# Performance work log

Measured on AMD Instinct MI355X. Metric: run time of the kernel, lower is better.

Reference implementation:

```python
import jax, jax.numpy as jnp
import numpy as np
from jax import lax

B, H, OUT, STEPS = 256, 512, 9, 325  # 1 initial step + 325 unrolled steps = 326 outputs


def setup_inputs() -> dict:
    key = jax.random.key(0)
    ks = jax.random.split(key, 12)
    s = 0.05
    return {
        "x": jax.random.normal(ks[0], (B, H), jnp.float32),
        "hx0": jax.random.normal(ks[1], (B, H), jnp.float32),
        "cx0": jax.random.normal(ks[2], (B, H), jnp.float32),
        "W_ih": jax.random.normal(ks[3], (4 * H, H), jnp.float32) * s,
        "W_hh": jax.random.normal(ks[4], (4 * H, H), jnp.float32) * s,
        "b_ih": jax.random.normal(ks[5], (4 * H,), jnp.float32) * s,
        "b_hh": jax.random.normal(ks[6], (4 * H,), jnp.float32) * s,
        "W1": jax.random.normal(ks[7], (H, H), jnp.float32) * s,
        "b1": jax.random.normal(ks[8], (H,), jnp.float32) * s,
        "W2": jax.random.normal(ks[9], (OUT, H), jnp.float32) * s,
        "b2": jax.random.normal(ks[10], (OUT,), jnp.float32) * s,
    }


def reference(x, hx0, cx0, W_ih, W_hh, b_ih, b_hh, W1, b1, W2, b2):
    def lstm_cell(inp, h, c):
        # PyTorch LSTMCell gate order: i, f, g, o
        gates = inp @ W_ih.T + b_ih + h @ W_hh.T + b_hh  # [B, 4H]
        i, f, g, o = jnp.split(gates, 4, axis=-1)
        i = jax.nn.sigmoid(i)
        f = jax.nn.sigmoid(f)
        g = jnp.tanh(g)
        o = jax.nn.sigmoid(o)
        c_new = f * c + i * g
        h_new = o * jnp.tanh(c_new)
        return h_new, c_new

    def mlp(h):
        return jax.nn.relu(h @ W1.T + b1) @ W2.T + b2  # [B, 9]

    h, c = lstm_cell(x, hx0, cx0)
    y0 = mlp(h)

    def step(carry, _):
        h, c = carry
        # original: self.cell(hx, (hx, cx)) -- input IS the current hidden state
        h, c = lstm_cell(h, h, c)
        return (h, c), mlp(h)

    _, ys = lax.scan(step, (h, c), None, length=STEPS)  # ys: [325, B, 9]
    out = jnp.concatenate([y0[None], ys], axis=0)  # [326, B, 9]
    return jnp.transpose(out, (1, 0, 2))  # [B, 326, 9]
```

## Files before the change

kernel.cpp:

```cpp
#include <hip/hip_runtime.h>
#include <cstdio>

#define B_   256
#define H_   512
#define G4_  2048
#define T_   326
#define OUT_ 9

typedef __attribute__((ext_vector_type(8))) short s16x8;
typedef __attribute__((ext_vector_type(4))) float f32x4;

__device__ inline unsigned short to_bf16(float f) {
    unsigned int u = __builtin_bit_cast(unsigned int, f);
    unsigned int r = (u + 0x7fffu + ((u >> 16) & 1u)) >> 16;
    return (unsigned short)r;
}

__device__ inline float sigmoidf_(float x) { return 1.0f / (1.0f + __expf(-x)); }

__device__ inline float fast_tanh(float x) {
    x = fminf(fmaxf(x, -15.f), 15.f);
    float e = __expf(2.f * x);
    return (e - 1.f) / (e + 1.f);
}


__global__ void prep_weights(const float* __restrict__ Wih, const float* __restrict__ Whh,
                             const float* __restrict__ bih, const float* __restrict__ bhh,
                             unsigned short* __restrict__ Wc, unsigned short* __restrict__ Wcat,
                             float* __restrict__ bc) {
    int idx = blockIdx.x * 256 + threadIdx.x;
    int n = idx >> 9, k = idx & 511;
    float wi = Wih[idx], wh = Whh[idx];
    Wc[idx] = to_bf16(wi + wh);
    Wcat[(n << 10) + k]       = to_bf16(wi);
    Wcat[(n << 10) + 512 + k] = to_bf16(wh);
    if (k == 0) bc[n] = bih[n] + bhh[n];
}

__global__ void prep_w1(const float* __restrict__ W1, unsigned short* __restrict__ W1b) {
    int idx = blockIdx.x * 256 + threadIdx.x;
    W1b[idx] = to_bf16(W1[idx]);
}

__global__ void prep_w2(const float* __restrict__ W2, unsigned short* __restrict__ W2b) {
    int idx = blockIdx.x * 256 + threadIdx.x;
    int o = idx >> 9, k = idx & 511;
    W2b[idx] = (o < OUT_) ? to_bf16(W2[o * H_ + k]) : (unsigned short)0;
}

__global__ void prep_x(const float* __restrict__ x, const float* __restrict__ hx0,
                       unsigned short* __restrict__ xcat) {
    int idx = blockIdx.x * 256 + threadIdx.x;
    int b = idx >> 9, k = idx & 511;
    xcat[(b << 10) + k]       = to_bf16(x[idx]);
    xcat[(b << 10) + 512 + k] = to_bf16(hx0[idx]);
}

template <int KLEN>
__global__ __launch_bounds__(256) void lstm_step(
    const unsigned short* __restrict__ A,
    const unsigned short* __restrict__ W,
    const float* __restrict__ bc,
    const float* __restrict__ c_in,
    float* __restrict__ c_out,
    unsigned short* __restrict__ h_out) {
    const int lane = threadIdx.x & 63;
    const int wave = threadIdx.x >> 6;
    const int mn = lane & 15, q = lane >> 4;
    const int rt = blockIdx.x & 15;
    const int hb = (blockIdx.x >> 4) * 64 + wave * 16;

    const unsigned short* ap  = A + (size_t)(rt * 16 + mn) * KLEN + q * 8;
    const unsigned short* wp0 = W + (size_t)(0 * H_ + hb + mn) * KLEN + q * 8;
    const unsigned short* wp1 = W + (size_t)(1 * H_ + hb + mn) * KLEN + q * 8;
    const unsigned short* wp2 = W + (size_t)(2 * H_ + hb + mn) * KLEN + q * 8;
    const unsigned short* wp3 = W + (size_t)(3 * H_ + hb + mn) * KLEN + q * 8;

    f32x4 acc0 = {0.f,0.f,0.f,0.f}, acc1 = {0.f,0.f,0.f,0.f};
    f32x4 acc2 = {0.f,0.f,0.f,0.f}, acc3 = {0.f,0.f,0.f,0.f};
#pragma unroll 4
    for (int k0 = 0; k0 < KLEN; k0 += 32) {
        s16x8 a  = *reinterpret_cast<const s16x8*>(ap + k0);
        s16x8 w0 = *reinterpret_cast<const s16x8*>(wp0 + k0);
        s16x8 w1 = *reinterpret_cast<const s16x8*>(wp1 + k0);
        s16x8 w2 = *reinterpret_cast<const s16x8*>(wp2 + k0);
        s16x8 w3 = *reinterpret_cast<const s16x8*>(wp3 + k0);
        acc0 = __builtin_amdgcn_mfma_f32_16x16x32_bf16(a, w0, acc0, 0, 0, 0);
        acc1 = __builtin_amdgcn_mfma_f32_16x16x32_bf16(a, w1, acc1, 0, 0, 0);
        acc2 = __builtin_amdgcn_mfma_f32_16x16x32_bf16(a, w2, acc2, 0, 0, 0);
        acc3 = __builtin_amdgcn_mfma_f32_16x16x32_bf16(a, w3, acc3, 0, 0, 0);
    }

    const int j = hb + mn;
    const float bi = bc[j], bfv = bc[H_ + j], bg = bc[2 * H_ + j], bo = bc[3 * H_ + j];
#pragma unroll
    for (int r = 0; r < 4; ++r) {
        const int row = rt * 16 + q * 4 + r;
        const float iv = sigmoidf_(acc0[r] + bi);
        const float fv = sigmoidf_(acc1[r] + bfv);
        const float gv = fast_tanh(acc2[r] + bg);
        const float ov = sigmoidf_(acc3[r] + bo);
        const float co = c_in[row * H_ + j];
        const float cn = fv * co + iv * gv;
        c_out[row * H_ + j] = cn;
        h_out[row * H_ + j] = to_bf16(ov * fast_tanh(cn));
    }
}

__global__ __launch_bounds__(256) void lstm_persist(
    const unsigned short* __restrict__ Wc,
    const float* __restrict__ bc,
    const float* __restrict__ c0,
    unsigned short* __restrict__ h_hist,
    unsigned int* __restrict__ ctr) {
    __shared__ unsigned short A_lds[16 * 512];
    __shared__ float gate_lds[4 * 16 * 33];
    const int tid = threadIdx.x;
    const int lane = tid & 63, wave = tid >> 6;
    const int mn = lane & 15, q = lane >> 4;
    const int g  = blockIdx.x & 15;
    const int jb = (blockIdx.x >> 4) * 32;
    unsigned int* ctr_g = ctr + g * 32;

    s16x8 breg[2][16];
#pragma unroll
    for (int n = 0; n < 2; ++n) {
        const unsigned short* wp = Wc + (size_t)(wave * H_ + jb + n * 16 + mn) * H_ + q * 8;
#pragma unroll
        for (int kk = 0; kk < 16; ++kk)
            breg[n][kk] = *reinterpret_cast<const s16x8*>(wp + kk * 32);
    }
    const float bcv0 = bc[wave * H_ + jb + mn];
    const float bcv1 = bc[wave * H_ + jb + 16 + mn];

    const int crow = tid >> 4, cc0 = (tid & 15) * 2;
    float c_x = c0[(size_t)(g * 16 + crow) * H_ + jb + cc0];
    float c_y = c0[(size_t)(g * 16 + crow) * H_ + jb + cc0 + 1];

    int a_st[8];
#pragma unroll
    for (int p = 0; p < 8; ++p) {
        const int qi = p * 256 + tid;
        const int row = qi >> 7;
        const int bcol = (qi & 127) * 8;
        a_st[p] = row * 512 + (((bcol) ^ ((row & 7) << 4)) >> 1);
    }
    int a_rd[16];
#pragma unroll
    for (int kk = 0; kk < 16; ++kk) {
        const int bcol = kk * 64 + q * 16;
        a_rd[kk] = mn * 512 + ((bcol ^ ((mn & 7) << 4)) >> 1);
    }

    for (int t = 1; t < T_; ++t) {
        const unsigned long long* hsrc64 = reinterpret_cast<const unsigned long long*>(
            h_hist + (size_t)(t - 1) * (B_ * H_) + (size_t)g * 16 * H_);
        unsigned long long vv[8];
#pragma unroll
        for (int p = 0; p < 8; ++p)
            vv[p] = __hip_atomic_load(hsrc64 + p * 256 + tid, __ATOMIC_RELAXED,
                                      __HIP_MEMORY_SCOPE_AGENT);
#pragma unroll
        for (int p = 0; p < 8; ++p)
            *reinterpret_cast<unsigned long long*>(&A_lds[a_st[p]]) = vv[p];
        __syncthreads();

        f32x4 acc0 = {0.f,0.f,0.f,0.f}, acc1 = {0.f,0.f,0.f,0.f};
#pragma unroll
        for (int kk = 0; kk < 16; ++kk) {
            s16x8 a = *reinterpret_cast<const s16x8*>(&A_lds[a_rd[kk]]);
            acc0 = __builtin_amdgcn_mfma_f32_16x16x32_bf16(a, breg[0][kk], acc0, 0, 0, 0);
            acc1 = __builtin_amdgcn_mfma_f32_16x16x32_bf16(a, breg[1][kk], acc1, 0, 0, 0);
        }

#pragma unroll
        for (int r = 0; r < 4; ++r) {
            float v0 = acc0[r] + bcv0, v1 = acc1[r] + bcv1;
            if (wave == 2) { v0 = fast_tanh(v0); v1 = fast_tanh(v1); }
            else           { v0 = sigmoidf_(v0); v1 = sigmoidf_(v1); }
            gate_lds[(wave * 16 + (q * 4 + r)) * 33 + mn]      = v0;
            gate_lds[(wave * 16 + (q * 4 + r)) * 33 + 16 + mn] = v1;
        }
        __syncthreads();

        {
            float iv0 = gate_lds[(0 * 16 + crow) * 33 + cc0], iv1 = gate_lds[(0 * 16 + crow) * 33 + cc0 + 1];
            float fv0 = gate_lds[(1 * 16 + crow) * 33 + cc0], fv1 = gate_lds[(1 * 16 + crow) * 33 + cc0 + 1];
            float gv0 = gate_lds[(2 * 16 + crow) * 33 + cc0], gv1 = gate_lds[(2 * 16 + crow) * 33 + cc0 + 1];
            float ov0 = gate_lds[(3 * 16 + crow) * 33 + cc0], ov1 = gate_lds[(3 * 16 + crow) * 33 + cc0 + 1];
            c_x = fv0 * c_x + iv0 * gv0;
            c_y = fv1 * c_y + iv1 * gv1;
            unsigned int h0 = to_bf16(ov0 * fast_tanh(c_x));
            unsigned int h1 = to_bf16(ov1 * fast_tanh(c_y));
            unsigned int packed = h0 | (h1 << 16);
            unsigned int* hdst = reinterpret_cast<unsigned int*>(
                h_hist + (size_t)t * (B_ * H_) + (size_t)(g * 16 + crow) * H_ + jb + cc0);
            __hip_atomic_store(hdst, packed, __ATOMIC_RELAXED, __HIP_MEMORY_SCOPE_AGENT);
        }

        if (t < T_ - 1) {
            __syncthreads();
            asm volatile("" ::: "memory");
            if (tid == 0) {
                __hip_atomic_fetch_add(ctr_g, 1u, __ATOMIC_RELAXED, __HIP_MEMORY_SCOPE_AGENT);
                const unsigned int target = 16u * (unsigned int)t;
                while (__hip_atomic_load(ctr_g, __ATOMIC_RELAXED, __HIP_MEMORY_SCOPE_AGENT) < target) {
                }
            }
            asm volatile("" ::: "memory");
            __syncthreads();
        }
    }
}

__global__ __launch_bounds__(256) void mlp_kernel(
    const unsigned short* __restrict__ h_hist,
    const unsigned short* __restrict__ W1b,
    const float* __restrict__ b1,
    const unsigned short* __restrict__ W2b,
    const float* __restrict__ b2,
    float* __restrict__ out) {
    constexpr int ZS = 520;
    __shared__ unsigned short z_lds[32 * ZS];

    const int lane = threadIdx.x & 63;
    const int wave = threadIdx.x >> 6;
    const int mn = lane & 15, q = lane >> 4;
    const int t = blockIdx.x >> 2, mt = blockIdx.x & 3;

    const unsigned short* Abase = h_hist + ((size_t)t * B_ + mt * 64) * H_;
    const int nb = wave * 128;

    f32x4 zero4 = {0.f,0.f,0.f,0.f};
    f32x4 acc[4][8];
#pragma unroll
    for (int m4 = 0; m4 < 4; ++m4)
#pragma unroll
        for (int nt = 0; nt < 8; ++nt) acc[m4][nt] = zero4;

    for (int k0 = 0; k0 < 512; k0 += 32) {
        s16x8 a[4];
#pragma unroll
        for (int m4 = 0; m4 < 4; ++m4)
            a[m4] = *reinterpret_cast<const s16x8*>(Abase + (size_t)(m4 * 16 + mn) * H_ + k0 + q * 8);
#pragma unroll
        for (int nt = 0; nt < 8; ++nt) {
            s16x8 b = *reinterpret_cast<const s16x8*>(W1b + (size_t)(nb + nt * 16 + mn) * H_ + k0 + q * 8);
#pragma unroll
            for (int m4 = 0; m4 < 4; ++m4)
                acc[m4][nt] = __builtin_amdgcn_mfma_f32_16x16x32_bf16(a[m4], b, acc[m4][nt], 0, 0, 0);
        }
    }

    float b1v[8];
#pragma unroll
    for (int nt = 0; nt < 8; ++nt) b1v[nt] = b1[nb + nt * 16 + mn];

    for (int pass = 0; pass < 2; ++pass) {
        __syncthreads();
#pragma unroll
        for (int m4i = 0; m4i < 2; ++m4i) {
            const int m4 = 2 * pass + m4i;
            const int rl = m4i * 16 + q * 4;
#pragma unroll
            for (int nt = 0; nt < 8; ++nt) {
                const int col = nb + nt * 16 + mn;
#pragma unroll
                for (int r = 0; r < 4; ++r) {
                    float v = acc[m4][nt][r] + b1v[nt];
                    v = v > 0.f ? v : 0.f;
                    z_lds[(rl + r) * ZS + col] = to_bf16(v);
                }
            }
        }
        __syncthreads();
        if (wave < 2) {
            f32x4 yacc = {0.f,0.f,0.f,0.f};
#pragma unroll 4
            for (int k0 = 0; k0 < 512; k0 += 32) {
                s16x8 az = *reinterpret_cast<const s16x8*>(&z_lds[(wave * 16 + mn) * ZS + k0 + q * 8]);
                s16x8 bw = *reinterpret_cast<const s16x8*>(W2b + (size_t)mn * H_ + k0 + q * 8);
                yacc = __builtin_amdgcn_mfma_f32_16x16x32_bf16(az, bw, yacc, 0, 0, 0);
            }
            if (mn < OUT_) {
                const float bias = b2[mn];
#pragma unroll
                for (int r = 0; r < 4; ++r) {
                    const int row_local = pass * 32 + wave * 16 + q * 4 + r;
                    const int b = mt * 64 + row_local;
                    out[(size_t)b * (T_ * OUT_) + t * OUT_ + mn] = yacc[r] + bias;
                }
            }
        }
    }
}

extern "C" void kernel_launch(void* const* d_in, const int* in_sizes, int n_in,
                              void* d_out, int out_size, void* d_ws, size_t ws_size,
                              hipStream_t stream) {
    (void)in_sizes; (void)n_in; (void)out_size;
    const float* x   = (const float*)d_in[0];
    const float* hx0 = (const float*)d_in[1];
    const float* cx0 = (const float*)d_in[2];
    const float* Wih = (const float*)d_in[3];
    const float* Whh = (const float*)d_in[4];
    const float* bih = (const float*)d_in[5];
    const float* bhh = (const float*)d_in[6];
    const float* W1  = (const float*)d_in[7];
    const float* b1  = (const float*)d_in[8];
    const float* W2  = (const float*)d_in[9];
    const float* b2  = (const float*)d_in[10];
    float* out = (float*)d_out;

    char* p = (char*)d_ws;
    size_t off = 0;
    auto alloc = [&](size_t bytes) {
        void* r = p + off;
        off = (off + bytes + 255) & ~(size_t)255;
        return r;
    };
    unsigned short* Wc     = (unsigned short*)alloc((size_t)G4_ * H_ * 2);
    unsigned short* Wcat   = (unsigned short*)alloc((size_t)G4_ * 1024 * 2);
    unsigned short* W1b    = (unsigned short*)alloc((size_t)H_ * H_ * 2);
    unsigned short* W2b    = (unsigned short*)alloc((size_t)16 * H_ * 2);
    float*          bc     = (float*)alloc((size_t)G4_ * 4);
    unsigned short* xcat   = (unsigned short*)alloc((size_t)B_ * 1024 * 2);
    float*          cbuf   = (float*)alloc((size_t)B_ * H_ * 4);
    unsigned int*   ctr    = (unsigned int*)alloc(4096);
    unsigned short* h_hist = (unsigned short*)alloc((size_t)T_ * B_ * H_ * 2);
    if (off > ws_size) {
        fprintf(stderr, "kernel_launch: ws too small: need %zu have %zu\n", off, ws_size);
        return;
    }

    prep_weights<<<G4_ * H_ / 256, 256, 0, stream>>>(Wih, Whh, bih, bhh, Wc, Wcat, bc);
    prep_w1<<<H_ * H_ / 256, 256, 0, stream>>>(W1, W1b);
    prep_w2<<<16 * H_ / 256, 256, 0, stream>>>(W2, W2b);
    prep_x<<<B_ * H_ / 256, 256, 0, stream>>>(x, hx0, xcat);

    lstm_step<1024><<<128, 256, 0, stream>>>(xcat, Wcat, bc, cx0, cbuf, h_hist);

    hipMemsetAsync(ctr, 0, 4096, stream);
    {
        const unsigned short* Wc_l = Wc;
        const float* bc_l = bc;
        const float* c0_l = cbuf;
        unsigned short* hh_l = h_hist;
        unsigned int* ctr_l = ctr;
        void* args[5] = {(void*)&Wc_l, (void*)&bc_l, (void*)&c0_l, (void*)&hh_l, (void*)&ctr_l};
        hipLaunchCooperativeKernel((const void*)lstm_persist, dim3(256), dim3(256), args, 0, stream);
    }

    mlp_kernel<<<T_ * 4, 256, 0, stream>>>(h_hist, W1b, b1, W2b, b2, out);
}
```

Before: 1.019 ms.

## Fuse MLP head into persistent LSTM kernel, overlapping it with the barrier wait

Removes the separate MLP kernel. Waves 2-3 of each persistent block keep a 32-column slice of W1 and W2 in registers. After each step's barrier they compute that slice of the MLP for the previous timestep from the h tile already staged in LDS. Partial outputs are combined with float atomicAdd into a zeroed workspace, and a small kernel then copies the result to the output. This hides MLP work inside the recurrence but adds per-step work on the critical path for two waves, plus many atomics. The launch also changes from cooperative to a normal launch.

```diff
diff --git a/kernel.cpp b/kernel.cpp
--- a/kernel.cpp
+++ b/kernel.cpp
@@ -9,6 +9,7 @@
 
 typedef __attribute__((ext_vector_type(8))) short s16x8;
 typedef __attribute__((ext_vector_type(4))) float f32x4;
+typedef unsigned long long ull;
 
 __device__ inline unsigned short to_bf16(float f) {
     unsigned int u = __builtin_bit_cast(unsigned int, f);
@@ -113,14 +114,21 @@
     const float* __restrict__ bc,
     const float* __restrict__ c0,
     unsigned short* __restrict__ h_hist,
-    unsigned int* __restrict__ ctr) {
+    unsigned int* __restrict__ ctr,
+    const unsigned short* __restrict__ W1b,
+    const float* __restrict__ b1,
+    const unsigned short* __restrict__ W2b,
+    const float* __restrict__ b2,
+    float* __restrict__ ws_y) {
     __shared__ unsigned short A_lds[16 * 512];
     __shared__ float gate_lds[4 * 16 * 33];
+    __shared__ unsigned short z_lds[2 * 16 * 24];
     const int tid = threadIdx.x;
     const int lane = tid & 63, wave = tid >> 6;
     const int mn = lane & 15, q = lane >> 4;
     const int g  = blockIdx.x & 15;
-    const int jb = (blockIdx.x >> 4) * 32;
+    const int wg = blockIdx.x >> 4;
+    const int jb = wg * 32;
     unsigned int* ctr_g = ctr + g * 32;
 
     s16x8 breg[2][16];
@@ -144,7 +152,7 @@
         const int qi = p * 256 + tid;
         const int row = qi >> 7;
         const int bcol = (qi & 127) * 8;
-        a_st[p] = row * 512 + (((bcol) ^ ((row & 7) << 4)) >> 1);
+        a_st[p] = row * 512 + ((bcol ^ ((row & 7) << 4)) >> 1);
     }
     int a_rd[16];
 #pragma unroll
@@ -153,17 +161,57 @@
         a_rd[kk] = mn * 512 + ((bcol ^ ((mn & 7) << 4)) >> 1);
     }
 
+    s16x8 w1reg[16];
+    s16x8 w2reg = {0,0,0,0,0,0,0,0};
+    float b1v = 0.f, b2v = 0.f;
+    const int zw = wave - 2;
+    if (wave >= 2) {
+        const int zbase = wg * 32 + zw * 16;
+        const unsigned short* wp = W1b + (size_t)(zbase + mn) * H_ + q * 8;
+#pragma unroll
+        for (int kk = 0; kk < 16; ++kk)
+            w1reg[kk] = *reinterpret_cast<const s16x8*>(wp + kk * 32);
+        b1v = b1[zbase + mn];
+        if (q < 2)
+            w2reg = *reinterpret_cast<const s16x8*>(W2b + (size_t)mn * H_ + zbase + q * 8);
+        b2v = (mn < OUT_ && wg == 0 && wave == 2) ? b2[mn] : 0.f;
+    }
+
+    auto mlp_pass = [&](int tout) {
+        f32x4 zacc = {0.f,0.f,0.f,0.f};
+#pragma unroll
+        for (int kk = 0; kk < 16; ++kk) {
+            s16x8 a = *reinterpret_cast<const s16x8*>(&A_lds[a_rd[kk]]);
+            zacc = __builtin_amdgcn_mfma_f32_16x16x32_bf16(a, w1reg[kk], zacc, 0, 0, 0);
+        }
+#pragma unroll
+        for (int r = 0; r < 4; ++r) {
+            float v = zacc[r] + b1v;
+            v = v > 0.f ? v : 0.f;
+            z_lds[zw * 384 + (q * 4 + r) * 24 + mn] = to_bf16(v);
+        }
+        s16x8 az = {0,0,0,0,0,0,0,0};
+        if (q < 2) az = *reinterpret_cast<const s16x8*>(&z_lds[zw * 384 + mn * 24 + q * 8]);
+        f32x4 y = __builtin_amdgcn_mfma_f32_16x16x32_bf16(az, w2reg, f32x4{0.f,0.f,0.f,0.f}, 0, 0, 0);
+        if (mn < OUT_) {
+#pragma unroll
+            for (int r = 0; r < 4; ++r)
+                atomicAdd(&ws_y[(size_t)(g * 16 + q * 4 + r) * (T_ * OUT_) + tout * OUT_ + mn],
+                          y[r] + b2v);
+        }
+    };
+
     for (int t = 1; t < T_; ++t) {
-        const unsigned long long* hsrc64 = reinterpret_cast<const unsigned long long*>(
+        const ull* hsrc64 = reinterpret_cast<const ull*>(
             h_hist + (size_t)(t - 1) * (B_ * H_) + (size_t)g * 16 * H_);
-        unsigned long long vv[8];
+        ull vv[8];
 #pragma unroll
         for (int p = 0; p < 8; ++p)
             vv[p] = __hip_atomic_load(hsrc64 + p * 256 + tid, __ATOMIC_RELAXED,
                                       __HIP_MEMORY_SCOPE_AGENT);
 #pragma unroll
         for (int p = 0; p < 8; ++p)
-            *reinterpret_cast<unsigned long long*>(&A_lds[a_st[p]]) = vv[p];
+            *reinterpret_cast<ull*>(&A_lds[a_st[p]]) = vv[p];
         __syncthreads();
 
         f32x4 acc0 = {0.f,0.f,0.f,0.f}, acc1 = {0.f,0.f,0.f,0.f};
@@ -199,101 +247,38 @@
             __hip_atomic_store(hdst, packed, __ATOMIC_RELAXED, __HIP_MEMORY_SCOPE_AGENT);
         }
 
-        if (t < T_ - 1) {
-            __syncthreads();
-            asm volatile("" ::: "memory");
-            if (tid == 0) {
-                __hip_atomic_fetch_add(ctr_g, 1u, __ATOMIC_RELAXED, __HIP_MEMORY_SCOPE_AGENT);
-                const unsigned int target = 16u * (unsigned int)t;
-                while (__hip_atomic_load(ctr_g, __ATOMIC_RELAXED, __HIP_MEMORY_SCOPE_AGENT) < target) {
-                }
+        __syncthreads();
+        asm volatile("" ::: "memory");
+        if (tid == 0) {
+            __hip_atomic_fetch_add(ctr_g, 1u, __ATOMIC_RELAXED, __HIP_MEMORY_SCOPE_AGENT);
+            const unsigned int target = 16u * (unsigned int)t;
+            while (__hip_atomic_load(ctr_g, __ATOMIC_RELAXED, __HIP_MEMORY_SCOPE_AGENT) < target) {
             }
-            asm volatile("" ::: "memory");
-            __syncthreads();
-        }
-    }
-}
-
-__global__ __launch_bounds__(256) void mlp_kernel(
-    const unsigned short* __restrict__ h_hist,
-    const unsigned short* __restrict__ W1b,
-    const float* __restrict__ b1,
-    const unsigned short* __restrict__ W2b,
-    const float* __restrict__ b2,
-    float* __restrict__ out) {
-    constexpr int ZS = 520;
-    __shared__ unsigned short z_lds[32 * ZS];
-
-    const int lane = threadIdx.x & 63;
-    const int wave = threadIdx.x >> 6;
-    const int mn = lane & 15, q = lane >> 4;
-    const int t = blockIdx.x >> 2, mt = blockIdx.x & 3;
-
-    const unsigned short* Abase = h_hist + ((size_t)t * B_ + mt * 64) * H_;
-    const int nb = wave * 128;
-
-    f32x4 zero4 = {0.f,0.f,0.f,0.f};
-    f32x4 acc[4][8];
-#pragma unroll
-    for (int m4 = 0; m4 < 4; ++m4)
-#pragma unroll
-        for (int nt = 0; nt < 8; ++nt) acc[m4][nt] = zero4;
-
-    for (int k0 = 0; k0 < 512; k0 += 32) {
-        s16x8 a[4];
-#pragma unroll
-        for (int m4 = 0; m4 < 4; ++m4)
-            a[m4] = *reinterpret_cast<const s16x8*>(Abase + (size_t)(m4 * 16 + mn) * H_ + k0 + q * 8);
-#pragma unroll
-        for (int nt = 0; nt < 8; ++nt) {
-            s16x8 b = *reinterpret_cast<const s16x8*>(W1b + (size_t)(nb + nt * 16 + mn) * H_ + k0 + q * 8);
-#pragma unroll
-            for (int m4 = 0; m4 < 4; ++m4)
-                acc[m4][nt] = __builtin_amdgcn_mfma_f32_16x16x32_bf16(a[m4], b, acc[m4][nt], 0, 0, 0);
-        }
-    }
-
-    float b1v[8];
-#pragma unroll
-    for (int nt = 0; nt < 8; ++nt) b1v[nt] = b1[nb + nt * 16 + mn];
-
-    for (int pass = 0; pass < 2; ++pass) {
-        __syncthreads();
-#pragma unroll
-        for (int m4i = 0; m4i < 2; ++m4i) {
-            const int m4 = 2 * pass + m4i;
-            const int rl = m4i * 16 + q * 4;
-#pragma unroll
-            for (int nt = 0; nt < 8; ++nt) {
-                const int col = nb + nt * 16 + mn;
-#pragma unroll
-                for (int r = 0; r < 4; ++r) {
-                    float v = acc[m4][nt][r] + b1v[nt];
-                    v = v > 0.f ? v : 0.f;
-                    z_lds[(rl + r) * ZS + col] = to_bf16(v);
-                }
-            }
-        }
-        __syncthreads();
-        if (wave < 2) {
-            f32x4 yacc = {0.f,0.f,0.f,0.f};
-#pragma unroll 4
-            for (int k0 = 0; k0 < 512; k0 += 32) {
-                s16x8 az = *reinterpret_cast<const s16x8*>(&z_lds[(wave * 16 + mn) * ZS + k0 + q * 8]);
-                s16x8 bw = *reinterpret_cast<const s16x8*>(W2b + (size_t)mn * H_ + k0 + q * 8);
-                yacc = __builtin_amdgcn_mfma_f32_16x16x32_bf16(az, bw, yacc, 0, 0, 0);
-            }
-            if (mn < OUT_) {
-                const float bias = b2[mn];
-#pragma unroll
-                for (int r = 0; r < 4; ++r) {
-                    const int row_local = pass * 32 + wave * 16 + q * 4 + r;
-                    const int b = mt * 64 + row_local;
-                    out[(size_t)b * (T_ * OUT_) + t * OUT_ + mn] = yacc[r] + bias;
-                }
-            }
-        }
-    }
+        }
+        if (wave >= 2) mlp_pass(t - 1);
+        asm volatile("" ::: "memory");
+        __syncthreads();
+    }
+
+    {
+        const ull* hsrc64 = reinterpret_cast<const ull*>(
+            h_hist + (size_t)(T_ - 1) * (B_ * H_) + (size_t)g * 16 * H_);
+        ull vv[8];
+#pragma unroll
+        for (int p = 0; p < 8; ++p)
+            vv[p] = __hip_atomic_load(hsrc64 + p * 256 + tid, __ATOMIC_RELAXED,
+                                      __HIP_MEMORY_SCOPE_AGENT);
+#pragma unroll
+        for (int p = 0; p < 8; ++p)
+            *reinterpret_cast<ull*>(&A_lds[a_st[p]]) = vv[p];
+        __syncthreads();
+        if (wave >= 2) mlp_pass(T_ - 1);
+    }
+}
+
+__global__ void copy_out(const float* __restrict__ ws_y, float* __restrict__ out) {
+    int idx = blockIdx.x * 256 + threadIdx.x;
+    out[idx] = ws_y[idx];
 }
 
 extern "C" void kernel_launch(void* const* d_in, const int* in_sizes, int n_in,
@@ -328,6 +313,7 @@
     unsigned short* xcat   = (unsigned short*)alloc((size_t)B_ * 1024 * 2);
     float*          cbuf   = (float*)alloc((size_t)B_ * H_ * 4);
     unsigned int*   ctr    = (unsigned int*)alloc(4096);
+    float*          ws_y   = (float*)alloc((size_t)B_ * T_ * OUT_ * 4);
     unsigned short* h_hist = (unsigned short*)alloc((size_t)T_ * B_ * H_ * 2);
     if (off > ws_size) {
         fprintf(stderr, "kernel_launch: ws too small: need %zu have %zu\n", off, ws_size);
@@ -342,15 +328,10 @@
     lstm_step<1024><<<128, 256, 0, stream>>>(xcat, Wcat, bc, cx0, cbuf, h_hist);
 
     hipMemsetAsync(ctr, 0, 4096, stream);
-    {
-        const unsigned short* Wc_l = Wc;
-        const float* bc_l = bc;
-        const float* c0_l = cbuf;
-        unsigned short* hh_l = h_hist;
-        unsigned int* ctr_l = ctr;
-        void* args[5] = {(void*)&Wc_l, (void*)&bc_l, (void*)&c0_l, (void*)&hh_l, (void*)&ctr_l};
-        hipLaunchCooperativeKernel((const void*)lstm_persist, dim3(256), dim3(256), args, 0, stream);
-    }
-
-    mlp_kernel<<<T_ * 4, 256, 0, stream>>>(h_hist, W1b, b1, W2b, b2, out);
-}
+    hipMemsetAsync(ws_y, 0, (size_t)B_ * T_ * OUT_ * 4, stream);
+
+    lstm_persist<<<256, 256, 0, stream>>>(Wc, bc, cbuf, h_hist, ctr,
+                                          W1b, b1, W2b, b2, ws_y);
+
+    copy_out<<<(B_ * T_ * OUT_) / 256, 256, 0, stream>>>(ws_y, out);
+}
```

After: 1.045 ms. 2.6% more time.

## Merge prep kernels and restructure MLP to stage h tiles through swizzled LDS

Applied to the files above, without the earlier changes.

Fuses the four weight/input conversion kernels into a single launch to cut launch overhead. In the MLP kernel, each 16-row slice of h is loaded cooperatively into an XOR-swizzled LDS tile and the first GEMM runs one m-tile at a time with 8 accumulators instead of 32. This reduces register pressure and uncoalesced global A reads. The cost is more barriers, and W1 B-fragments are re-read from global memory once per m-tile.

```diff
diff --git a/kernel.cpp b/kernel.cpp
--- a/kernel.cpp
+++ b/kernel.cpp
@@ -9,6 +9,7 @@
 
 typedef __attribute__((ext_vector_type(8))) short s16x8;
 typedef __attribute__((ext_vector_type(4))) float f32x4;
+typedef unsigned long long ull;
 
 __device__ inline unsigned short to_bf16(float f) {
     unsigned int u = __builtin_bit_cast(unsigned int, f);
@@ -24,37 +25,35 @@
     return (e - 1.f) / (e + 1.f);
 }
 
-
-__global__ void prep_weights(const float* __restrict__ Wih, const float* __restrict__ Whh,
-                             const float* __restrict__ bih, const float* __restrict__ bhh,
-                             unsigned short* __restrict__ Wc, unsigned short* __restrict__ Wcat,
-                             float* __restrict__ bc) {
-    int idx = blockIdx.x * 256 + threadIdx.x;
-    int n = idx >> 9, k = idx & 511;
-    float wi = Wih[idx], wh = Whh[idx];
-    Wc[idx] = to_bf16(wi + wh);
-    Wcat[(n << 10) + k]       = to_bf16(wi);
-    Wcat[(n << 10) + 512 + k] = to_bf16(wh);
-    if (k == 0) bc[n] = bih[n] + bhh[n];
-}
-
-__global__ void prep_w1(const float* __restrict__ W1, unsigned short* __restrict__ W1b) {
-    int idx = blockIdx.x * 256 + threadIdx.x;
-    W1b[idx] = to_bf16(W1[idx]);
-}
-
-__global__ void prep_w2(const float* __restrict__ W2, unsigned short* __restrict__ W2b) {
-    int idx = blockIdx.x * 256 + threadIdx.x;
-    int o = idx >> 9, k = idx & 511;
-    W2b[idx] = (o < OUT_) ? to_bf16(W2[o * H_ + k]) : (unsigned short)0;
-}
-
-__global__ void prep_x(const float* __restrict__ x, const float* __restrict__ hx0,
-                       unsigned short* __restrict__ xcat) {
-    int idx = blockIdx.x * 256 + threadIdx.x;
-    int b = idx >> 9, k = idx & 511;
-    xcat[(b << 10) + k]       = to_bf16(x[idx]);
-    xcat[(b << 10) + 512 + k] = to_bf16(hx0[idx]);
+__global__ void prep_all(const float* __restrict__ Wih, const float* __restrict__ Whh,
+                         const float* __restrict__ bih, const float* __restrict__ bhh,
+                         const float* __restrict__ W1, const float* __restrict__ W2,
+                         const float* __restrict__ x, const float* __restrict__ hx0,
+                         unsigned short* __restrict__ Wc, unsigned short* __restrict__ Wcat,
+                         float* __restrict__ bc, unsigned short* __restrict__ W1b,
+                         unsigned short* __restrict__ W2b, unsigned short* __restrict__ xcat) {
+    const int b = blockIdx.x;
+    if (b < 4096) {
+        int idx = b * 256 + threadIdx.x;
+        int n = idx >> 9, k = idx & 511;
+        float wi = Wih[idx], wh = Whh[idx];
+        Wc[idx] = to_bf16(wi + wh);
+        Wcat[(n << 10) + k]       = to_bf16(wi);
+        Wcat[(n << 10) + 512 + k] = to_bf16(wh);
+        if (k == 0) bc[n] = bih[n] + bhh[n];
+    } else if (b < 4096 + 1024) {
+        int idx = (b - 4096) * 256 + threadIdx.x;
+        W1b[idx] = to_bf16(W1[idx]);
+    } else if (b < 4096 + 1024 + 32) {
+        int idx = (b - 5120) * 256 + threadIdx.x;
+        int o = idx >> 9, k = idx & 511;
+        W2b[idx] = (o < OUT_) ? to_bf16(W2[o * H_ + k]) : (unsigned short)0;
+    } else {
+        int idx = (b - 5152) * 256 + threadIdx.x;
+        int bb = idx >> 9, k = idx & 511;
+        xcat[(bb << 10) + k]       = to_bf16(x[idx]);
+        xcat[(bb << 10) + 512 + k] = to_bf16(hx0[idx]);
+    }
 }
 
 template <int KLEN>
@@ -144,7 +143,7 @@
         const int qi = p * 256 + tid;
         const int row = qi >> 7;
         const int bcol = (qi & 127) * 8;
-        a_st[p] = row * 512 + (((bcol) ^ ((row & 7) << 4)) >> 1);
+        a_st[p] = row * 512 + ((bcol ^ ((row & 7) << 4)) >> 1);
     }
     int a_rd[16];
 #pragma unroll
@@ -154,16 +153,16 @@
     }
 
     for (int t = 1; t < T_; ++t) {
-        const unsigned long long* hsrc64 = reinterpret_cast<const unsigned long long*>(
+        const ull* hsrc64 = reinterpret_cast<const ull*>(
             h_hist + (size_t)(t - 1) * (B_ * H_) + (size_t)g * 16 * H_);
-        unsigned long long vv[8];
+        ull vv[8];
 #pragma unroll
         for (int p = 0; p < 8; ++p)
             vv[p] = __hip_atomic_load(hsrc64 + p * 256 + tid, __ATOMIC_RELAXED,
                                       __HIP_MEMORY_SCOPE_AGENT);
 #pragma unroll
         for (int p = 0; p < 8; ++p)
-            *reinterpret_cast<unsigned long long*>(&A_lds[a_st[p]]) = vv[p];
+            *reinterpret_cast<ull*>(&A_lds[a_st[p]]) = vv[p];
         __syncthreads();
 
         f32x4 acc0 = {0.f,0.f,0.f,0.f}, acc1 = {0.f,0.f,0.f,0.f};
@@ -222,35 +221,29 @@
     const float* __restrict__ b2,
     float* __restrict__ out) {
     constexpr int ZS = 520;
+    __shared__ unsigned short A_lds[16 * 512];
     __shared__ unsigned short z_lds[32 * ZS];
 
-    const int lane = threadIdx.x & 63;
-    const int wave = threadIdx.x >> 6;
+    const int tid = threadIdx.x;
+    const int lane = tid & 63;
+    const int wave = tid >> 6;
     const int mn = lane & 15, q = lane >> 4;
     const int t = blockIdx.x >> 2, mt = blockIdx.x & 3;
-
-    const unsigned short* Abase = h_hist + ((size_t)t * B_ + mt * 64) * H_;
     const int nb = wave * 128;
 
-    f32x4 zero4 = {0.f,0.f,0.f,0.f};
-    f32x4 acc[4][8];
-#pragma unroll
-    for (int m4 = 0; m4 < 4; ++m4)
-#pragma unroll
-        for (int nt = 0; nt < 8; ++nt) acc[m4][nt] = zero4;
-
-    for (int k0 = 0; k0 < 512; k0 += 32) {
-        s16x8 a[4];
-#pragma unroll
-        for (int m4 = 0; m4 < 4; ++m4)
-            a[m4] = *reinterpret_cast<const s16x8*>(Abase + (size_t)(m4 * 16 + mn) * H_ + k0 + q * 8);
-#pragma unroll
-        for (int nt = 0; nt < 8; ++nt) {
-            s16x8 b = *reinterpret_cast<const s16x8*>(W1b + (size_t)(nb + nt * 16 + mn) * H_ + k0 + q * 8);
-#pragma unroll
-            for (int m4 = 0; m4 < 4; ++m4)
-                acc[m4][nt] = __builtin_amdgcn_mfma_f32_16x16x32_bf16(a[m4], b, acc[m4][nt], 0, 0, 0);
-        }
+    int a_st[8];
+#pragma unroll
+    for (int p = 0; p < 8; ++p) {
+        const int qi = p * 256 + tid;
+        const int row = qi >> 7;
+        const int bcol = (qi & 127) * 8;
+        a_st[p] = row * 512 + ((bcol ^ ((row & 7) << 4)) >> 1);
+    }
+    int a_rd[16];
+#pragma unroll
+    for (int kk = 0; kk < 16; ++kk) {
+        const int bcol = kk * 64 + q * 16;
+        a_rd[kk] = mn * 512 + ((bcol ^ ((mn & 7) << 4)) >> 1);
     }
 
     float b1v[8];
@@ -258,23 +251,48 @@
     for (int nt = 0; nt < 8; ++nt) b1v[nt] = b1[nb + nt * 16 + mn];
 
     for (int pass = 0; pass < 2; ++pass) {
-        __syncthreads();
 #pragma unroll
         for (int m4i = 0; m4i < 2; ++m4i) {
             const int m4 = 2 * pass + m4i;
+            __syncthreads();
+            {
+                const ull* hsrc64 = reinterpret_cast<const ull*>(
+                    h_hist + ((size_t)t * B_ + mt * 64 + m4 * 16) * H_);
+                ull vv[8];
+#pragma unroll
+                for (int p = 0; p < 8; ++p) vv[p] = hsrc64[p * 256 + tid];
+#pragma unroll
+                for (int p = 0; p < 8; ++p)
+                    *reinterpret_cast<ull*>(&A_lds[a_st[p]]) = vv[p];
+            }
+            __syncthreads();
+
+            f32x4 acc[8];
+#pragma unroll
+            for (int nt = 0; nt < 8; ++nt) acc[nt] = f32x4{0.f,0.f,0.f,0.f};
+            for (int kk = 0; kk < 16; ++kk) {
+                s16x8 a = *reinterpret_cast<const s16x8*>(&A_lds[a_rd[kk]]);
+#pragma unroll
+                for (int nt = 0; nt < 8; ++nt) {
+                    s16x8 b = *reinterpret_cast<const s16x8*>(
+                        W1b + (size_t)(nb + nt * 16 + mn) * H_ + kk * 32 + q * 8);
+                    acc[nt] = __builtin_amdgcn_mfma_f32_16x16x32_bf16(a, b, acc[nt], 0, 0, 0);
+                }
+            }
             const int rl = m4i * 16 + q * 4;
 #pragma unroll
             for (int nt = 0; nt < 8; ++nt) {
                 const int col = nb + nt * 16 + mn;
 #pragma unroll
                 for (int r = 0; r < 4; ++r) {
-                    float v = acc[m4][nt][r] + b1v[nt];
+                    float v = acc[nt][r] + b1v[nt];
                     v = v > 0.f ? v : 0.f;
                     z_lds[(rl + r) * ZS + col] = to_bf16(v);
                 }
             }
         }
         __syncthreads();
+
         if (wave < 2) {
             f32x4 yacc = {0.f,0.f,0.f,0.f};
 #pragma unroll 4
@@ -334,10 +352,8 @@
         return;
     }
 
-    prep_weights<<<G4_ * H_ / 256, 256, 0, stream>>>(Wih, Whh, bih, bhh, Wc, Wcat, bc);
-    prep_w1<<<H_ * H_ / 256, 256, 0, stream>>>(W1, W1b);
-    prep_w2<<<16 * H_ / 256, 256, 0, stream>>>(W2, W2b);
-    prep_x<<<B_ * H_ / 256, 256, 0, stream>>>(x, hx0, xcat);
+    prep_all<<<5664, 256, 0, stream>>>(Wih, Whh, bih, bhh, W1, W2, x, hx0,
+                                       Wc, Wcat, bc, W1b, W2b, xcat);
 
     lstm_step<1024><<<128, 256, 0, stream>>>(xcat, Wcat, bc, cx0, cbuf, h_hist);
 
```

After: 1.536 ms. +50.7%, slower.
